# Kernel tuning notes

Hardware: AMD Instinct MI355X
Metric: run time of the kernel (lower is better)

## Reference

```python
import jax, jax.numpy as jnp
import numpy as np

B, G, D, N_HEADS, FFN, L = 16, 2048, 256, 8, 1024, 4
HEAD_DIM = D // N_HEADS
EPS_LN = 1e-5
MASK_TOKEN = -10.0
REE_BASE = 100.0


def setup_inputs() -> dict:
    key = jax.random.key(0)
    ks = jax.random.split(key, 20)
    s = 0.02
    inp = {
        'x': jax.random.normal(ks[0], (B, G), jnp.float32),
        'gene_emb': jax.random.normal(ks[1], (G, D), jnp.float32) * s,
        'inv_freq': (1.0 / REE_BASE ** (jnp.arange(0, D, 2, dtype=jnp.float32) / D)),
        'Wq': jax.random.normal(ks[2], (L, D, D), jnp.float32) * s,
        'bq': jnp.zeros((L, D), jnp.float32),
        'Wk': jax.random.normal(ks[3], (L, D, D), jnp.float32) * s,
        'bk': jnp.zeros((L, D), jnp.float32),
        'Wv': jax.random.normal(ks[4], (L, D, D), jnp.float32) * s,
        'bv': jnp.zeros((L, D), jnp.float32),
        'ln1_g': jnp.ones((L, D), jnp.float32),
        'ln1_b': jnp.zeros((L, D), jnp.float32),
        'ln2_g': jnp.ones((L, D), jnp.float32),
        'ln2_b': jnp.zeros((L, D), jnp.float32),
        'WU': jax.random.normal(ks[5], (L, D, FFN), jnp.float32) * s,
        'bU': jnp.zeros((L, FFN), jnp.float32),
        'WV': jax.random.normal(ks[6], (L, FFN, D), jnp.float32) * s,
        'bV': jnp.zeros((L, D), jnp.float32),
        'Wout': jax.random.normal(ks[7], (D, 1), jnp.float32) * s,
        'bout': jnp.zeros((1,), jnp.float32),
    }
    return inp


def layernorm(x, g, b):
    m = x.mean(-1, keepdims=True)
    v = ((x - m) ** 2).mean(-1, keepdims=True)
    return (x - m) / jnp.sqrt(v + EPS_LN) * g + b


def causal_linear_attention(q, k, v):
    # q, k already feature-mapped ('sqr'); shapes [B, S, H, dh]
    b, s, h, dh = q.shape
    qs, ks_, vs = (jnp.moveaxis(t, 1, 0) for t in (q, k, v))  # [S,B,H,dh]
    num0 = jnp.zeros((b, h, dh, dh), q.dtype)
    den0 = jnp.zeros((b, h, dh), q.dtype)

    def step(carry, qkv):
        num_s, den_s = carry
        qt, kt, vt = qkv
        num_s = num_s + jnp.einsum('bhf,bhd->bhfd', kt, vt)
        den_s = den_s + kt
        num = jnp.einsum('bhf,bhfd->bhd', qt, num_s)
        den = jnp.einsum('bhf,bhf->bh', qt, den_s)
        return (num_s, den_s), num / (den[..., None] + 1e-16)

    _, out = jax.lax.scan(step, (num0, den0), (qs, ks_, vs))  # [S,B,H,dh]
    return jnp.moveaxis(out, 0, 1).reshape(b, s, h * dh)


def reference(x, gene_emb, inv_freq, Wq, bq, Wk, bk, Wv, bv,
              ln1_g, ln1_b, ln2_g, ln2_b, WU, bU, WV, bV, Wout, bout):
    b, g = x.shape
    # Rotary Expression Embedding
    freqs = x[..., None] * inv_freq  # [B,G,D/2]
    emb = jnp.concatenate([jnp.sin(freqs), jnp.cos(freqs)], axis=-1)  # [B,G,D]
    emb = jnp.where((x == MASK_TOKEN)[..., None], 0.0, emb)
    h = gene_emb[None] + emb  # [B,G,D]

    for l in range(Wq.shape[0]):
        hn = layernorm(h, ln1_g[l], ln1_b[l])  # pre-LN (on_gptln=True)
        q = (hn @ Wq[l] + bq[l]).reshape(b, g, N_HEADS, HEAD_DIM) ** 2
        k = (hn @ Wk[l] + bk[l]).reshape(b, g, N_HEADS, HEAD_DIM) ** 2
        v = (hn @ Wv[l] + bv[l]).reshape(b, g, N_HEADS, HEAD_DIM)
        h = h + causal_linear_attention(q, k, v)
        hn2 = layernorm(h, ln2_g[l], ln2_b[l])
        h = h + jax.nn.gelu(hn2 @ WU[l] + bU[l], approximate=False) @ WV[l] + bV[l]
    return (h @ Wout + bout).squeeze(-1)  # [B,G]
```

## Files before the change

kernel.cpp:

```cpp
#include <hip/hip_runtime.h>
#include <math.h>


#define GG 2048
#define DD 256
#define NROWS 32768
#define NC 32
#define CS 64

typedef __attribute__((ext_vector_type(8))) short bf16x8;
typedef __attribute__((ext_vector_type(4))) float f32x4;

struct FalseT { static constexpr bool value = false; };
struct TrueT  { static constexpr bool value = true;  };

__device__ __forceinline__ short f2bf(float f) {
  union { float f; unsigned u; } v; v.f = f;
  unsigned r = v.u + 0x7FFFu + ((v.u >> 16) & 1u);
  return (short)(r >> 16);
}
__device__ __forceinline__ float bf2f(short s) {
  union { unsigned u; float f; } v; v.u = ((unsigned)(unsigned short)s) << 16;
  return v.f;
}
__device__ __forceinline__ void gld16(const short* g, short* l) {
  __builtin_amdgcn_global_load_lds(
      (const __attribute__((address_space(1))) void*)g,
      (__attribute__((address_space(3))) void*)l, 16, 0, 0);
}
__device__ __forceinline__ float fast_gelu(float x) {
  float y = 1.595769122f * (x + 0.044715f * x * x * x);
  return x / (1.0f + __expf(-y));
}

__global__ __launch_bounds__(256) void embed_kernel(
    const float* __restrict__ x, const float* __restrict__ ge,
    const float* __restrict__ invf, float* __restrict__ h) {
  int bg = blockIdx.x * 4 + (threadIdx.x >> 6);
  int g = bg & (GG - 1);
  int lane = threadIdx.x & 63;
  float xv = x[bg];
  int d = lane * 4;
  float4 e;
  if (lane < 32) {
    float4 f = *(const float4*)&invf[d];
    e.x = sinf(xv * f.x); e.y = sinf(xv * f.y);
    e.z = sinf(xv * f.z); e.w = sinf(xv * f.w);
  } else {
    float4 f = *(const float4*)&invf[d - 128];
    e.x = cosf(xv * f.x); e.y = cosf(xv * f.y);
    e.z = cosf(xv * f.z); e.w = cosf(xv * f.w);
  }
  if (xv == -10.0f) { e.x = 0.f; e.y = 0.f; e.z = 0.f; e.w = 0.f; }
  float4 gv = *(const float4*)&ge[(size_t)g * DD + d];
  float4 o; o.x = gv.x + e.x; o.y = gv.y + e.y; o.z = gv.z + e.z; o.w = gv.w + e.w;
  *(float4*)&h[(size_t)bg * DD + d] = o;
}

__global__ __launch_bounds__(256) void ln_tiled(
    const float* __restrict__ h, const float* __restrict__ gamma,
    const float* __restrict__ beta, short* __restrict__ outT) {
  __shared__ float mean_s[32], rstd_s[32];
  __shared__ float gls[256], bls[256];
  int r0 = blockIdx.x * 32;
  int tid = threadIdx.x;
  gls[tid] = gamma[tid]; bls[tid] = beta[tid];
  {
    int row = tid >> 3, seg = tid & 7;
    const float4* hp = (const float4*)(h + (size_t)(r0 + row) * DD + seg * 32);
    float s = 0.f, s2 = 0.f;
#pragma unroll
    for (int i = 0; i < 8; ++i) {
      float4 v = hp[i];
      s += v.x + v.y + v.z + v.w;
      s2 += v.x * v.x + v.y * v.y + v.z * v.z + v.w * v.w;
    }
    s += __shfl_xor(s, 1); s += __shfl_xor(s, 2); s += __shfl_xor(s, 4);
    s2 += __shfl_xor(s2, 1); s2 += __shfl_xor(s2, 2); s2 += __shfl_xor(s2, 4);
    if (seg == 0) {
      float mn = s * (1.0f / 256.0f);
      mean_s[row] = mn;
      rstd_s[row] = rsqrtf(s2 * (1.0f / 256.0f) - mn * mn + 1e-5f);
    }
  }
  __syncthreads();
  int row = tid & 31, kc8 = (tid >> 5) & 3, half = tid >> 7;
  float mn = mean_s[row], rs = rstd_s[row];
  size_t hrow = (size_t)(r0 + row) * DD;
  int trow = (r0 & 127) + row;
  short* tb = outT + (size_t)(r0 >> 7) * 8 * 4096 + (kc8 * 128 + trow) * 8;
#pragma unroll
  for (int j = 0; j < 4; ++j) {
    int kb = half * 4 + j;
    int k0 = kb * 32 + kc8 * 8;
    float4 x0 = *(const float4*)&h[hrow + k0];
    float4 x1 = *(const float4*)&h[hrow + k0 + 4];
    float4 g0 = *(const float4*)&gls[k0], g1 = *(const float4*)&gls[k0 + 4];
    float4 b0 = *(const float4*)&bls[k0], b1 = *(const float4*)&bls[k0 + 4];
    bf16x8 aw;
    aw[0] = f2bf((x0.x - mn) * rs * g0.x + b0.x);
    aw[1] = f2bf((x0.y - mn) * rs * g0.y + b0.y);
    aw[2] = f2bf((x0.z - mn) * rs * g0.z + b0.z);
    aw[3] = f2bf((x0.w - mn) * rs * g0.w + b0.w);
    aw[4] = f2bf((x1.x - mn) * rs * g1.x + b1.x);
    aw[5] = f2bf((x1.y - mn) * rs * g1.y + b1.y);
    aw[6] = f2bf((x1.z - mn) * rs * g1.z + b1.z);
    aw[7] = f2bf((x1.w - mn) * rs * g1.w + b1.w);
    *(bf16x8*)&tb[(size_t)kb * 4096] = aw;
  }
}

__global__ __launch_bounds__(256) void prep_weights(
    const float* __restrict__ Wq, const float* __restrict__ Wk,
    const float* __restrict__ Wv, const float* __restrict__ WU,
    const float* __restrict__ WV,
    short* __restrict__ TQ, short* __restrict__ TK, short* __restrict__ TV,
    short* __restrict__ TU, short* __restrict__ TVd) {
  int zz = blockIdx.z, l = blockIdx.y;
  const float* src; short* dst; int Kd, Nd;
  if (zz == 0) { src = Wq; dst = TQ; Kd = 256; Nd = 256; }
  else if (zz == 1) { src = Wk; dst = TK; Kd = 256; Nd = 256; }
  else if (zz == 2) { src = Wv; dst = TV; Kd = 256; Nd = 256; }
  else if (zz == 3) { src = WU; dst = TU; Kd = 256; Nd = 1024; }
  else { src = WV; dst = TVd; Kd = 1024; Nd = 256; }
  int tot = Kd * Nd;
  int e = blockIdx.x * 256 + threadIdx.x;
  if (e >= tot) return;
  int t = e >> 12;
  int cslot = (e >> 3) & 511;
  int elem = e & 7;
  int kc8 = cslot >> 7, rn = cslot & 127;
  int nKb = Kd >> 5;
  int nt = t / nKb, kb = t - nt * nKb;
  int n = nt * 128 + rn, k = kb * 32 + kc8 * 8 + elem;
  dst[(size_t)l * tot + e] = f2bf(src[(size_t)l * tot + (size_t)k * Nd + n]);
}

template <int K, int EPI>
__global__ __launch_bounds__(256) void gemm_t(
    const short* __restrict__ A, const short* __restrict__ B0,
    const short* __restrict__ B1, const short* __restrict__ B2,
    const float* __restrict__ bias0, const float* __restrict__ bias1,
    const float* __restrict__ bias2,
    short* __restrict__ o0, short* __restrict__ o1, short* __restrict__ o2,
    float* __restrict__ outf, int N) {
  __shared__ __align__(16) short L[24576];
  constexpr int nIter = K / 32;
  int z = blockIdx.z;
  const short* Bt = (z == 0) ? B0 : (z == 1) ? B1 : B2;
  const float* bias = (z == 0) ? bias0 : (z == 1) ? bias1 : bias2;
  short* outz = (z == 0) ? o0 : (z == 1) ? o1 : o2;
  int m0 = blockIdx.x * 128, n0 = blockIdx.y * 128;
  int tid = threadIdx.x;
  int lane = tid & 63, w = tid >> 6;
  int q = lane >> 4, r = lane & 15;
  int wm = (w >> 1) * 64, wn = (w & 1) * 64;
  const short* At = A + (size_t)blockIdx.x * nIter * 4096;
  const short* Btl = Bt + (size_t)blockIdx.y * nIter * 4096;
  f32x4 vzero = {0.f, 0.f, 0.f, 0.f};
  f32x4 acc[4][4];
#pragma unroll
  for (int i = 0; i < 4; ++i)
#pragma unroll
    for (int j = 0; j < 4; ++j) acc[i][j] = vzero;

  int c0 = tid * 8, c1 = (tid + 256) * 8;
#pragma unroll
  for (int g = 0; g < 3; ++g) {
    gld16(At + g * 4096 + c0, &L[g * 4096 + c0]);
    gld16(At + g * 4096 + c1, &L[g * 4096 + c1]);
    gld16(Btl + g * 4096 + c0, &L[12288 + g * 4096 + c0]);
    gld16(Btl + g * 4096 + c1, &L[12288 + g * 4096 + c1]);
  }

  int abase = (q * 128 + wm + r) * 8;
  int bbase = (q * 128 + wn + r) * 8;

#pragma unroll
  for (int gi = 0; gi < nIter; ++gi) {
    const int rem = nIter - 1 - gi;
    if (rem >= 2)      __builtin_amdgcn_s_waitcnt(0x0f78);
    else if (rem == 1) __builtin_amdgcn_s_waitcnt(0x0f74);
    else               __builtin_amdgcn_s_waitcnt(0x0f70);
    __builtin_amdgcn_s_barrier();
    const int cur = gi % 3;
    const short* Asc = &L[cur * 4096];
    const short* Bsc = &L[12288 + cur * 4096];
    bf16x8 af[4], bfr[4];
#pragma unroll
    for (int mt = 0; mt < 4; ++mt)
      af[mt] = *(const bf16x8*)&Asc[abase + mt * 16 * 8];
#pragma unroll
    for (int nt = 0; nt < 4; ++nt)
      bfr[nt] = *(const bf16x8*)&Bsc[bbase + nt * 16 * 8];
#pragma unroll
    for (int mt = 0; mt < 4; ++mt)
#pragma unroll
      for (int nt = 0; nt < 4; ++nt)
        acc[mt][nt] = __builtin_amdgcn_mfma_f32_16x16x32_bf16(bfr[nt], af[mt], acc[mt][nt], 0, 0, 0);
    __builtin_amdgcn_s_waitcnt(0xc07f);
    __builtin_amdgcn_s_barrier();
    if (gi + 3 < nIter) {
      size_t kn = (size_t)(gi + 3) * 4096;
      gld16(At + kn + c0, &L[cur * 4096 + c0]);
      gld16(At + kn + c1, &L[cur * 4096 + c1]);
      gld16(Btl + kn + c0, &L[12288 + cur * 4096 + c0]);
      gld16(Btl + kn + c1, &L[12288 + cur * 4096 + c1]);
    }
  }

  float4 bias4[4];
#pragma unroll
  for (int nt = 0; nt < 4; ++nt) bias4[nt] = *(const float4*)&bias[n0 + wn + nt * 16 + q * 4];

  if (EPI == 0) {
    short* T = L;
#pragma unroll
    for (int mt = 0; mt < 4; ++mt) {
      int ml = wm + mt * 16 + r;
#pragma unroll
      for (int nt = 0; nt < 4; ++nt) {
        f32x4 v = acc[mt][nt];
        v[0] += bias4[nt].x; v[1] += bias4[nt].y; v[2] += bias4[nt].z; v[3] += bias4[nt].w;
        if (z < 2) { v[0] *= v[0]; v[1] *= v[1]; v[2] *= v[2]; v[3] *= v[3]; }
        short4 pk; pk.x = f2bf(v[0]); pk.y = f2bf(v[1]); pk.z = f2bf(v[2]); pk.w = f2bf(v[3]);
        *(short4*)&T[ml * 132 + wn + nt * 16 + q * 4] = pk;
      }
    }
    __syncthreads();
#pragma unroll
    for (int t2 = 0; t2 < 2; ++t2) {
      int task = tid + t2 * 256;
      int row = task & 127, hl = task >> 7;
      size_t obase = ((size_t)((n0 >> 5) + hl) * NROWS + m0 + row) * 32;
#pragma unroll
      for (int j = 0; j < 4; ++j)
        *(bf16x8*)&outz[obase + j * 8] = *(const bf16x8*)&T[row * 132 + hl * 32 + j * 8];
    }
  } else if (EPI == 1) {
#pragma unroll
    for (int mt = 0; mt < 4; ++mt) {
      int ml = wm + mt * 16 + r;
#pragma unroll
      for (int nt = 0; nt < 4; ++nt) {
        f32x4 v = acc[mt][nt];
        v[0] += bias4[nt].x; v[1] += bias4[nt].y; v[2] += bias4[nt].z; v[3] += bias4[nt].w;
#pragma unroll
        for (int e = 0; e < 4; ++e) v[e] = fast_gelu(v[e]);
        short4 o; o.x = f2bf(v[0]); o.y = f2bf(v[1]); o.z = f2bf(v[2]); o.w = f2bf(v[3]);
        int n = n0 + wn + nt * 16 + q * 4;
        size_t ti = ((size_t)blockIdx.x * (N >> 5) + (n >> 5)) * 4096 +
                    (size_t)(((n >> 3) & 3) << 10) + (ml << 3) + (n & 7);
        *(short4*)&outz[ti] = o;
      }
    }
  } else {
    float* TF = (float*)L;
#pragma unroll
    for (int half = 0; half < 2; ++half) {
      __syncthreads();
      if ((w & 1) == half) {
#pragma unroll
        for (int mt = 0; mt < 4; ++mt) {
          int ml = wm + mt * 16 + r;
#pragma unroll
          for (int nt = 0; nt < 4; ++nt) {
            f32x4 v = acc[mt][nt];
            v[0] += bias4[nt].x; v[1] += bias4[nt].y; v[2] += bias4[nt].z; v[3] += bias4[nt].w;
            *(f32x4*)&TF[ml * 68 + nt * 16 + q * 4] = v;
          }
        }
      }
      __syncthreads();
      int row = tid >> 1, col = (tid & 1) * 32;
      size_t hoff = (size_t)(m0 + row) * N + n0 + half * 64 + col;
#pragma unroll
      for (int j = 0; j < 8; ++j) {
        float4 add = *(const float4*)&TF[row * 68 + col + j * 4];
        float4 cur4 = *(float4*)&outf[hoff + j * 4];
        cur4.x += add.x; cur4.y += add.y; cur4.z += add.z; cur4.w += add.w;
        *(float4*)&outf[hoff + j * 4] = cur4;
      }
    }
  }
}

__global__ __launch_bounds__(512) void ffn_fused(
    const short* __restrict__ A, const short* __restrict__ TUw,
    const short* __restrict__ TVw, const float* __restrict__ bUp,
    const float* __restrict__ bVp, float* __restrict__ h) {
  __shared__ __align__(16) short L[75776];
  float* BU = (float*)&L[73728];
  int tid = threadIdx.x;
  int lane = tid & 63, w = tid >> 6;
  int q = lane >> 4, r = lane & 15;
  int wmU = (w >> 1) * 32, wnU = (w & 1) * 64;
  int wmD = (w >> 2) * 64, wnD = (w & 3) * 64;
  int c16 = tid * 8;
  const short* At = A + (size_t)blockIdx.x * 32768;

  if (tid < 256) *(float4*)&BU[tid * 4] = *(const float4*)&bUp[tid * 4];

#pragma unroll
  for (int i = 0; i < 8; ++i) gld16(At + i * 4096 + c16, &L[i * 4096 + c16]);

  auto issueUp = [&](int ss, int jj, int buf) {
    short* dst = &L[49152 + buf * 8192];
    const short* g0 = TUw + ((size_t)ss * 8 + jj * 2) * 4096;
    gld16(g0 + c16, dst + c16);
    gld16(g0 + 4096 + c16, dst + 4096 + c16);
  };
  auto issueDown = [&](int ss, int ii, int buf) {
    short* dst = &L[49152 + buf * 8192];
    gld16(TVw + (size_t)(ss * 4 + ii) * 4096 + c16, dst + c16);
    gld16(TVw + (size_t)(32 + ss * 4 + ii) * 4096 + c16, dst + 4096 + c16);
  };

  issueUp(0, 0, 0); issueUp(0, 1, 1); issueUp(0, 2, 2);

  __builtin_amdgcn_s_waitcnt(0x0f76);
  __builtin_amdgcn_s_barrier();

  bf16x8 aR[8][2];
#pragma unroll
  for (int kb = 0; kb < 8; ++kb)
#pragma unroll
    for (int mt = 0; mt < 2; ++mt)
      aR[kb][mt] = *(const bf16x8*)&L[kb * 4096 + (q * 128 + wmU + mt * 16 + r) * 8];

  f32x4 vzero = {0.f, 0.f, 0.f, 0.f};
  f32x4 accm[2][4], acco[4][4];
#pragma unroll
  for (int mt = 0; mt < 2; ++mt)
#pragma unroll
    for (int nt = 0; nt < 4; ++nt) accm[mt][nt] = vzero;
#pragma unroll
  for (int mt = 0; mt < 4; ++mt)
#pragma unroll
    for (int nt = 0; nt < 4; ++nt) acco[mt][nt] = vzero;

  int cur = 0;

  auto slice = [&](int s, auto lastc) {
    constexpr bool LAST = decltype(lastc)::value;
#pragma unroll
    for (int j = 0; j < 4; ++j) {
      __builtin_amdgcn_s_waitcnt(0x0f74);
      __builtin_amdgcn_s_barrier();
      const short* Ws = &L[49152 + cur * 8192];
#pragma unroll
      for (int kk = 0; kk < 2; ++kk) {
        bf16x8 bfr[4];
#pragma unroll
        for (int nt = 0; nt < 4; ++nt)
          bfr[nt] = *(const bf16x8*)&Ws[kk * 4096 + (q * 128 + wnU + nt * 16 + r) * 8];
#pragma unroll
        for (int mt = 0; mt < 2; ++mt)
#pragma unroll
          for (int nt = 0; nt < 4; ++nt)
            accm[mt][nt] = __builtin_amdgcn_mfma_f32_16x16x32_bf16(
                bfr[nt], aR[j * 2 + kk][mt], accm[mt][nt], 0, 0, 0);
      }
      if (j == 3) {
        float4 b4[4];
#pragma unroll
        for (int nt = 0; nt < 4; ++nt)
          b4[nt] = *(const float4*)&BU[s * 128 + wnU + nt * 16 + q * 4];
#pragma unroll
        for (int mt = 0; mt < 2; ++mt) {
          int row = wmU + mt * 16 + r;
#pragma unroll
          for (int nt = 0; nt < 4; ++nt) {
            f32x4 v = accm[mt][nt];
            v[0] += b4[nt].x; v[1] += b4[nt].y; v[2] += b4[nt].z; v[3] += b4[nt].w;
            short4 pk;
            pk.x = f2bf(fast_gelu(v[0])); pk.y = f2bf(fast_gelu(v[1]));
            pk.z = f2bf(fast_gelu(v[2])); pk.w = f2bf(fast_gelu(v[3]));
            int f0 = wnU + nt * 16 + q * 4;
            *(short4*)&L[32768 + (f0 >> 5) * 4096 +
                         (((f0 >> 3) & 3) * 128 + row) * 8 + (f0 & 7)] = pk;
            accm[mt][nt] = vzero;
          }
        }
      }
      __builtin_amdgcn_s_waitcnt(0xc07f);
      __builtin_amdgcn_s_barrier();
      if (j == 0) issueUp(s, 3, cur);
      else issueDown(s, j - 1, cur);
      cur = (cur == 2) ? 0 : cur + 1;
    }
#pragma unroll
    for (int i = 0; i < 4; ++i) {
      if (LAST && i == 2)      __builtin_amdgcn_s_waitcnt(0x0f72);
      else if (LAST && i == 3) __builtin_amdgcn_s_waitcnt(0x0f70);
      else                     __builtin_amdgcn_s_waitcnt(0x0f74);
      __builtin_amdgcn_s_barrier();
      const short* Ws = &L[49152 + cur * 8192];
      bf16x8 am[4], bvf[4];
#pragma unroll
      for (int mt = 0; mt < 4; ++mt)
        am[mt] = *(const bf16x8*)&L[32768 + i * 4096 + (q * 128 + wmD + mt * 16 + r) * 8];
#pragma unroll
      for (int nt = 0; nt < 4; ++nt)
        bvf[nt] = *(const bf16x8*)&Ws[(wnD >> 7) * 4096 + (q * 128 + (wnD & 127) + nt * 16 + r) * 8];
#pragma unroll
      for (int mt = 0; mt < 4; ++mt)
#pragma unroll
        for (int nt = 0; nt < 4; ++nt)
          acco[mt][nt] = __builtin_amdgcn_mfma_f32_16x16x32_bf16(bvf[nt], am[mt], acco[mt][nt], 0, 0, 0);
      __builtin_amdgcn_s_waitcnt(0xc07f);
      __builtin_amdgcn_s_barrier();
      if (i == 0) issueDown(s, 3, cur);
      else if (!LAST) issueUp(s + 1, i - 1, cur);
      cur = (cur == 2) ? 0 : cur + 1;
    }
  };

  for (int s = 0; s < 7; ++s) slice(s, FalseT{});
  slice(7, TrueT{});

  float4 bv4[4];
#pragma unroll
  for (int nt = 0; nt < 4; ++nt) bv4[nt] = *(const float4*)&bVp[wnD + nt * 16 + q * 4];
  float* TF = (float*)L;
#pragma unroll
  for (int mt = 0; mt < 4; ++mt) {
    int row = wmD + mt * 16 + r;
#pragma unroll
    for (int nt = 0; nt < 4; ++nt) {
      f32x4 v = acco[mt][nt];
      v[0] += bv4[nt].x; v[1] += bv4[nt].y; v[2] += bv4[nt].z; v[3] += bv4[nt].w;
      *(f32x4*)&TF[row * 260 + wnD + nt * 16 + q * 4] = v;
    }
  }
  __syncthreads();
  size_t hbase = ((size_t)blockIdx.x * 128 + w * 16) * DD;
#pragma unroll
  for (int j = 0; j < 16; ++j) {
    float4 add = *(const float4*)&TF[(w * 16 + j) * 260 + lane * 4];
    float4 c4 = *(float4*)&h[hbase + (size_t)j * DD + lane * 4];
    c4.x += add.x; c4.y += add.y; c4.z += add.z; c4.w += add.w;
    *(float4*)&h[hbase + (size_t)j * DD + lane * 4] = c4;
  }
}

__global__ __launch_bounds__(256) void attn_chunk_kv(
    const short* __restrict__ Kb, const short* __restrict__ Vb,
    float* __restrict__ St, float* __restrict__ Zc) {
  __shared__ short Kt[4][32 * 72];
  __shared__ short Vt[4][32 * 72];
  int wid = threadIdx.x >> 6;
  int blk = blockIdx.x * 4 + wid;
  int c = blk & (NC - 1), bh = blk >> 5;
  int b = bh >> 3, hh = bh & 7;
  int lane = threadIdx.x & 63, q = lane >> 4, r = lane & 15;
  size_t rowbase = ((size_t)hh * NROWS + b * GG + c * CS + lane) * 32;
#pragma unroll
  for (int j = 0; j < 4; ++j) {
    bf16x8 kv = *(const bf16x8*)&Kb[rowbase + j * 8];
    bf16x8 vv = *(const bf16x8*)&Vb[rowbase + j * 8];
#pragma unroll
    for (int e = 0; e < 8; ++e) {
      Kt[wid][(j * 8 + e) * 72 + lane] = kv[e];
      Vt[wid][(j * 8 + e) * 72 + lane] = vv[e];
    }
  }
  __syncthreads();
  f32x4 vzero = {0.f, 0.f, 0.f, 0.f};
  f32x4 acc[2][2];
#pragma unroll
  for (int i = 0; i < 2; ++i)
#pragma unroll
    for (int j = 0; j < 2; ++j) acc[i][j] = vzero;
#pragma unroll
  for (int ks = 0; ks < 2; ++ks) {
    bf16x8 afr[2], bfr[2];
#pragma unroll
    for (int mt = 0; mt < 2; ++mt) afr[mt] = *(const bf16x8*)&Kt[wid][(mt * 16 + r) * 72 + ks * 32 + q * 8];
#pragma unroll
    for (int nt = 0; nt < 2; ++nt) bfr[nt] = *(const bf16x8*)&Vt[wid][(nt * 16 + r) * 72 + ks * 32 + q * 8];
#pragma unroll
    for (int mt = 0; mt < 2; ++mt)
#pragma unroll
      for (int nt = 0; nt < 2; ++nt)
        acc[mt][nt] = __builtin_amdgcn_mfma_f32_16x16x32_bf16(afr[mt], bfr[nt], acc[mt][nt], 0, 0, 0);
  }
  float* stp = St + ((size_t)bh * NC + c) * 1024;
#pragma unroll
  for (int mt = 0; mt < 2; ++mt)
#pragma unroll
    for (int nt = 0; nt < 2; ++nt)
      *(f32x4*)&stp[(nt * 16 + r) * 32 + mt * 16 + q * 4] = acc[mt][nt];
  if (lane < 32) {
    float s = 0.f;
#pragma unroll
    for (int j = 0; j < 8; ++j) {
      bf16x8 kr = *(const bf16x8*)&Kt[wid][lane * 72 + j * 8];
#pragma unroll
      for (int e = 0; e < 8; ++e) s += bf2f(kr[e]);
    }
    Zc[((size_t)bh * NC + c) * 32 + lane] = s;
  }
}

__global__ __launch_bounds__(1024) void attn_prefix(float* __restrict__ St, float* __restrict__ Zc) {
  int bh = blockIdx.x, i = threadIdx.x;
  float run = 0.f;
  float* p = St + (size_t)bh * NC * 1024 + i;
#pragma unroll
  for (int c = 0; c < NC; ++c) { float t = p[(size_t)c * 1024]; p[(size_t)c * 1024] = run; run += t; }
  if (i < 32) {
    float rz = 0.f;
    float* pz = Zc + (size_t)bh * NC * 32 + i;
#pragma unroll
    for (int c = 0; c < NC; ++c) { float t = pz[c * 32]; pz[c * 32] = rz; rz += t; }
  }
}

__global__ __launch_bounds__(256) void attn_intra(
    const short* __restrict__ Qb, const short* __restrict__ Kb,
    const short* __restrict__ Vb, const float* __restrict__ St,
    const float* __restrict__ Zc, float* __restrict__ h) {
  __shared__ short P[4][64 * 72];
  __shared__ short Vt[4][32 * 72];
  __shared__ float den[4][64];
  int wid = threadIdx.x >> 6;
  int blk = blockIdx.x * 4 + wid;
  int c = blk & (NC - 1), bh = blk >> 5;
  int b = bh >> 3, hh = bh & 7;
  int lane = threadIdx.x & 63, q = lane >> 4, r = lane & 15;
  size_t hrow0 = (size_t)b * GG + c * CS;
  size_t qrow0 = (size_t)hh * NROWS + b * GG + c * CS;

  const float* zp = Zc + ((size_t)bh * NC + c) * 32;
  float qz = 0.f;
  {
    size_t qoff = (qrow0 + lane) * 32;
#pragma unroll
    for (int j = 0; j < 4; ++j) {
      bf16x8 qv = *(const bf16x8*)&Qb[qoff + j * 8];
#pragma unroll
      for (int e = 0; e < 8; ++e) qz += bf2f(qv[e]) * zp[j * 8 + e];
    }
  }
  den[wid][lane] = qz;

  {
    size_t voff = (qrow0 + lane) * 32;
#pragma unroll
    for (int j = 0; j < 4; ++j) {
      bf16x8 vv = *(const bf16x8*)&Vb[voff + j * 8];
#pragma unroll
      for (int e = 0; e < 8; ++e) Vt[wid][(j * 8 + e) * 72 + lane] = vv[e];
    }
  }

  bf16x8 ak[4], bqf[4];
#pragma unroll
  for (int t4 = 0; t4 < 4; ++t4) {
    ak[t4]  = *(const bf16x8*)&Kb[(qrow0 + t4 * 16 + r) * 32 + q * 8];
    bqf[t4] = *(const bf16x8*)&Qb[(qrow0 + t4 * 16 + r) * 32 + q * 8];
  }
  f32x4 vzero = {0.f, 0.f, 0.f, 0.f};
  f32x4 pacc[4][4];
#pragma unroll
  for (int mt = 0; mt < 4; ++mt)
#pragma unroll
    for (int nt = 0; nt < 4; ++nt)
      pacc[mt][nt] = __builtin_amdgcn_mfma_f32_16x16x32_bf16(ak[mt], bqf[nt], vzero, 0, 0, 0);

  float rs[4] = {0.f, 0.f, 0.f, 0.f};
#pragma unroll
  for (int nt = 0; nt < 4; ++nt) {
    int t = nt * 16 + r;
#pragma unroll
    for (int mt = 0; mt < 4; ++mt) {
      short4 pk;
#pragma unroll
      for (int rr = 0; rr < 4; ++rr) {
        int s = mt * 16 + q * 4 + rr;
        float pv = (s <= t) ? pacc[mt][nt][rr] : 0.f;
        rs[nt] += pv;
        ((short*)&pk)[rr] = f2bf(pv);
      }
      *(short4*)&P[wid][t * 72 + mt * 16 + q * 4] = pk;
    }
  }
#pragma unroll
  for (int nt = 0; nt < 4; ++nt) {
    rs[nt] += __shfl_xor(rs[nt], 16);
    rs[nt] += __shfl_xor(rs[nt], 32);
  }
  __syncthreads();
  if (lane < 16) {
#pragma unroll
    for (int nt = 0; nt < 4; ++nt) den[wid][nt * 16 + lane] += rs[nt];
  }
  __syncthreads();

  f32x4 oacc[4][2];
#pragma unroll
  for (int mt = 0; mt < 4; ++mt)
#pragma unroll
    for (int nt2 = 0; nt2 < 2; ++nt2) oacc[mt][nt2] = vzero;
  const float* stp = St + ((size_t)bh * NC + c) * 1024;
#pragma unroll
  for (int nt2 = 0; nt2 < 2; ++nt2) {
    float4 s0 = *(const float4*)&stp[(nt2 * 16 + r) * 32 + q * 8];
    float4 s1 = *(const float4*)&stp[(nt2 * 16 + r) * 32 + q * 8 + 4];
    bf16x8 bs;
    bs[0] = f2bf(s0.x); bs[1] = f2bf(s0.y); bs[2] = f2bf(s0.z); bs[3] = f2bf(s0.w);
    bs[4] = f2bf(s1.x); bs[5] = f2bf(s1.y); bs[6] = f2bf(s1.z); bs[7] = f2bf(s1.w);
#pragma unroll
    for (int mt = 0; mt < 4; ++mt)
      oacc[mt][nt2] = __builtin_amdgcn_mfma_f32_16x16x32_bf16(bqf[mt], bs, oacc[mt][nt2], 0, 0, 0);
  }
#pragma unroll
  for (int ks = 0; ks < 2; ++ks) {
    bf16x8 ap[4];
#pragma unroll
    for (int mt = 0; mt < 4; ++mt)
      ap[mt] = *(const bf16x8*)&P[wid][(mt * 16 + r) * 72 + ks * 32 + q * 8];
#pragma unroll
    for (int nt2 = 0; nt2 < 2; ++nt2) {
      bf16x8 bv_ = *(const bf16x8*)&Vt[wid][(nt2 * 16 + r) * 72 + ks * 32 + q * 8];
#pragma unroll
      for (int mt = 0; mt < 4; ++mt)
        oacc[mt][nt2] = __builtin_amdgcn_mfma_f32_16x16x32_bf16(ap[mt], bv_, oacc[mt][nt2], 0, 0, 0);
    }
  }

#pragma unroll
  for (int mt = 0; mt < 4; ++mt) {
#pragma unroll
    for (int rr = 0; rr < 4; ++rr) {
      int t = mt * 16 + q * 4 + rr;
      float inv = 1.0f / (den[wid][t] + 1e-16f);
#pragma unroll
      for (int nt2 = 0; nt2 < 2; ++nt2) {
        int d = nt2 * 16 + r;
        size_t off = (hrow0 + t) * DD + hh * 32 + d;
        h[off] += oacc[mt][nt2][rr] * inv;
      }
    }
  }
}

__global__ __launch_bounds__(256) void out_proj(
    const float* __restrict__ h, const float* __restrict__ Wout,
    const float* __restrict__ bout, float* __restrict__ out) {
  int row = blockIdx.x * 4 + (threadIdx.x >> 6);
  int lane = threadIdx.x & 63;
  float4 a = *(const float4*)&h[(size_t)row * DD + lane * 4];
  float4 w = *(const float4*)&Wout[lane * 4];
  float s = a.x * w.x + a.y * w.y + a.z * w.z + a.w * w.w;
#pragma unroll
  for (int o = 1; o < 64; o <<= 1) s += __shfl_xor(s, o);
  if (lane == 0) out[row] = s + bout[0];
}

extern "C" void kernel_launch(void* const* d_in, const int* in_sizes, int n_in,
                              void* d_out, int out_size, void* d_ws, size_t ws_size,
                              hipStream_t stream) {
  const float* x    = (const float*)d_in[0];
  const float* ge   = (const float*)d_in[1];
  const float* invf = (const float*)d_in[2];
  const float* Wq   = (const float*)d_in[3];
  const float* bq   = (const float*)d_in[4];
  const float* Wk   = (const float*)d_in[5];
  const float* bk   = (const float*)d_in[6];
  const float* Wv   = (const float*)d_in[7];
  const float* bv   = (const float*)d_in[8];
  const float* ln1g = (const float*)d_in[9];
  const float* ln1b = (const float*)d_in[10];
  const float* ln2g = (const float*)d_in[11];
  const float* ln2b = (const float*)d_in[12];
  const float* WU   = (const float*)d_in[13];
  const float* bU   = (const float*)d_in[14];
  const float* WV   = (const float*)d_in[15];
  const float* bV   = (const float*)d_in[16];
  const float* Wout = (const float*)d_in[17];
  const float* bout = (const float*)d_in[18];
  float* out = (float*)d_out;

  char* ws = (char*)d_ws;
  float* h   = (float*)(ws + 0);
  short* hn  = (short*)(ws + 33554432);
  char*  R   = ws + 50331648;
  short* qb  = (short*)(R + 0);
  short* kb  = (short*)(R + 16777216);
  short* vb  = (short*)(R + 33554432);
  float* St  = (float*)(R + 50331648);
  float* Zc  = (float*)(R + 67108864);
  char*  WT  = R + 67633152;
  short* TQ  = (short*)(WT + 0);
  short* TK  = (short*)(WT + 524288);
  short* TVq = (short*)(WT + 1048576);
  short* TU  = (short*)(WT + 1572864);
  short* TVd = (short*)(WT + 3670016);

  prep_weights<<<dim3(1024, 4, 5), 256, 0, stream>>>(Wq, Wk, Wv, WU, WV, TQ, TK, TVq, TU, TVd);
  embed_kernel<<<NROWS / 4, 256, 0, stream>>>(x, ge, invf, h);

  for (int l = 0; l < 4; ++l) {
    ln_tiled<<<NROWS / 32, 256, 0, stream>>>(h, ln1g + l * 256, ln1b + l * 256, hn);
    gemm_t<256, 0><<<dim3(256, 2, 3), 256, 0, stream>>>(
        hn, TQ + l * 65536, TK + l * 65536, TVq + l * 65536,
        bq + l * 256, bk + l * 256, bv + l * 256,
        qb, kb, vb, nullptr, 256);
    attn_chunk_kv<<<1024, 256, 0, stream>>>(kb, vb, St, Zc);
    attn_prefix<<<128, 1024, 0, stream>>>(St, Zc);
    attn_intra<<<1024, 256, 0, stream>>>(qb, kb, vb, St, Zc, h);
    ln_tiled<<<NROWS / 32, 256, 0, stream>>>(h, ln2g + l * 256, ln2b + l * 256, hn);
    ffn_fused<<<256, 512, 0, stream>>>(hn, TU + l * 262144, TVd + l * 262144,
                                       bU + l * 1024, bV + l * 256, h);
  }
  out_proj<<<NROWS / 4, 256, 0, stream>>>(h, Wout, bout, out);
}
```

Measured before the change: 753.8 us.

## Split fused FFN into 64-row blocks of 256 threads with smaller LDS

The fused FFN kernel now processes 64 rows per block with 4 waves instead of 128 rows with 8 waves, launching 512 blocks instead of 256. Activations are loaded straight from global memory into registers instead of being staged through LDS, and the LDS footprint drops from about 148KB to about 68KB. This should allow more blocks per CU and fill all CUs, but each weight slice is now streamed twice as often per row processed. Each wave also holds a larger 2x8 down-projection tile, which raises register pressure.

```diff
diff --git a/kernel.cpp b/kernel.cpp
--- a/kernel.cpp
+++ b/kernel.cpp
@@ -285,59 +285,60 @@
   }
 }
 
-__global__ __launch_bounds__(512) void ffn_fused(
+__global__ __launch_bounds__(256) void ffn_fused(
     const short* __restrict__ A, const short* __restrict__ TUw,
     const short* __restrict__ TVw, const float* __restrict__ bUp,
     const float* __restrict__ bVp, float* __restrict__ h) {
-  __shared__ __align__(16) short L[75776];
-  float* BU = (float*)&L[73728];
+  __shared__ __align__(16) short L[34816];
+  float* BU = (float*)&L[32768];
   int tid = threadIdx.x;
   int lane = tid & 63, w = tid >> 6;
   int q = lane >> 4, r = lane & 15;
   int wmU = (w >> 1) * 32, wnU = (w & 1) * 64;
-  int wmD = (w >> 2) * 64, wnD = (w & 3) * 64;
-  int c16 = tid * 8;
-  const short* At = A + (size_t)blockIdx.x * 32768;
-
-  if (tid < 256) *(float4*)&BU[tid * 4] = *(const float4*)&bUp[tid * 4];
-
-#pragma unroll
-  for (int i = 0; i < 8; ++i) gld16(At + i * 4096 + c16, &L[i * 4096 + c16]);
+  int wmD = (w >> 1) * 32, wnD = (w & 1) * 128;
+  const short* At = A + (size_t)(blockIdx.x >> 1) * 32768;
+  int rbase = (blockIdx.x & 1) * 64;
+
+  *(float4*)&BU[tid * 4] = *(const float4*)&bUp[tid * 4];
+
+  bf16x8 aR[8][2];
+#pragma unroll
+  for (int kb = 0; kb < 8; ++kb)
+#pragma unroll
+    for (int mt = 0; mt < 2; ++mt)
+      aR[kb][mt] = *(const bf16x8*)&At[kb * 4096 + (q * 128 + rbase + wmU + mt * 16 + r) * 8];
+
+  __builtin_amdgcn_s_waitcnt(0x0f70);
 
   auto issueUp = [&](int ss, int jj, int buf) {
-    short* dst = &L[49152 + buf * 8192];
+    short* dst = &L[8192 + buf * 8192];
     const short* g0 = TUw + ((size_t)ss * 8 + jj * 2) * 4096;
-    gld16(g0 + c16, dst + c16);
-    gld16(g0 + 4096 + c16, dst + 4096 + c16);
+#pragma unroll
+    for (int i = 0; i < 4; ++i)
+      gld16(g0 + (i * 256 + tid) * 8, dst + (i * 256 + tid) * 8);
   };
   auto issueDown = [&](int ss, int ii, int buf) {
-    short* dst = &L[49152 + buf * 8192];
-    gld16(TVw + (size_t)(ss * 4 + ii) * 4096 + c16, dst + c16);
-    gld16(TVw + (size_t)(32 + ss * 4 + ii) * 4096 + c16, dst + 4096 + c16);
+    short* dst = &L[8192 + buf * 8192];
+    const short* gA = TVw + (size_t)(ss * 4 + ii) * 4096;
+    const short* gB = TVw + (size_t)(32 + ss * 4 + ii) * 4096;
+#pragma unroll
+    for (int i = 0; i < 2; ++i) {
+      gld16(gA + (i * 256 + tid) * 8, dst + (i * 256 + tid) * 8);
+      gld16(gB + (i * 256 + tid) * 8, dst + 4096 + (i * 256 + tid) * 8);
+    }
   };
 
   issueUp(0, 0, 0); issueUp(0, 1, 1); issueUp(0, 2, 2);
 
-  __builtin_amdgcn_s_waitcnt(0x0f76);
-  __builtin_amdgcn_s_barrier();
-
-  bf16x8 aR[8][2];
-#pragma unroll
-  for (int kb = 0; kb < 8; ++kb)
-#pragma unroll
-    for (int mt = 0; mt < 2; ++mt)
-      aR[kb][mt] = *(const bf16x8*)&L[kb * 4096 + (q * 128 + wmU + mt * 16 + r) * 8];
-
   f32x4 vzero = {0.f, 0.f, 0.f, 0.f};
-  f32x4 accm[2][4], acco[4][4];
-#pragma unroll
-  for (int mt = 0; mt < 2; ++mt)
+  f32x4 accm[2][4], acco[2][8];
+#pragma unroll
+  for (int mt = 0; mt < 2; ++mt) {
 #pragma unroll
     for (int nt = 0; nt < 4; ++nt) accm[mt][nt] = vzero;
 #pragma unroll
-  for (int mt = 0; mt < 4; ++mt)
-#pragma unroll
-    for (int nt = 0; nt < 4; ++nt) acco[mt][nt] = vzero;
+    for (int nt = 0; nt < 8; ++nt) acco[mt][nt] = vzero;
+  }
 
   int cur = 0;
 
@@ -345,9 +346,9 @@
     constexpr bool LAST = decltype(lastc)::value;
 #pragma unroll
     for (int j = 0; j < 4; ++j) {
-      __builtin_amdgcn_s_waitcnt(0x0f74);
+      __builtin_amdgcn_s_waitcnt(0x0f78);
       __builtin_amdgcn_s_barrier();
-      const short* Ws = &L[49152 + cur * 8192];
+      const short* Ws = &L[8192 + cur * 8192];
 #pragma unroll
       for (int kk = 0; kk < 2; ++kk) {
         bf16x8 bfr[4];
@@ -377,8 +378,7 @@
             pk.x = f2bf(fast_gelu(v[0])); pk.y = f2bf(fast_gelu(v[1]));
             pk.z = f2bf(fast_gelu(v[2])); pk.w = f2bf(fast_gelu(v[3]));
             int f0 = wnU + nt * 16 + q * 4;
-            *(short4*)&L[32768 + (f0 >> 5) * 4096 +
-                         (((f0 >> 3) & 3) * 128 + row) * 8 + (f0 & 7)] = pk;
+            *(short4*)&L[(f0 >> 5) * 2048 + (((f0 >> 3) & 3) * 64 + row) * 8 + (f0 & 7)] = pk;
             accm[mt][nt] = vzero;
           }
         }
@@ -391,22 +391,22 @@
     }
 #pragma unroll
     for (int i = 0; i < 4; ++i) {
-      if (LAST && i == 2)      __builtin_amdgcn_s_waitcnt(0x0f72);
+      if (LAST && i == 2)      __builtin_amdgcn_s_waitcnt(0x0f74);
       else if (LAST && i == 3) __builtin_amdgcn_s_waitcnt(0x0f70);
-      else                     __builtin_amdgcn_s_waitcnt(0x0f74);
+      else                     __builtin_amdgcn_s_waitcnt(0x0f78);
       __builtin_amdgcn_s_barrier();
-      const short* Ws = &L[49152 + cur * 8192];
-      bf16x8 am[4], bvf[4];
-#pragma unroll
-      for (int mt = 0; mt < 4; ++mt)
-        am[mt] = *(const bf16x8*)&L[32768 + i * 4096 + (q * 128 + wmD + mt * 16 + r) * 8];
-#pragma unroll
-      for (int nt = 0; nt < 4; ++nt)
+      const short* Ws = &L[8192 + cur * 8192];
+      bf16x8 am[2], bvf[8];
+#pragma unroll
+      for (int mt = 0; mt < 2; ++mt)
+        am[mt] = *(const bf16x8*)&L[i * 2048 + (q * 64 + wmD + mt * 16 + r) * 8];
+#pragma unroll
+      for (int nt = 0; nt < 8; ++nt)
         bvf[nt] = *(const bf16x8*)&Ws[(wnD >> 7) * 4096 + (q * 128 + (wnD & 127) + nt * 16 + r) * 8];
 #pragma unroll
-      for (int mt = 0; mt < 4; ++mt)
-#pragma unroll
-        for (int nt = 0; nt < 4; ++nt)
+      for (int mt = 0; mt < 2; ++mt)
+#pragma unroll
+        for (int nt = 0; nt < 8; ++nt)
           acco[mt][nt] = __builtin_amdgcn_mfma_f32_16x16x32_bf16(bvf[nt], am[mt], acco[mt][nt], 0, 0, 0);
       __builtin_amdgcn_s_waitcnt(0xc07f);
       __builtin_amdgcn_s_barrier();
@@ -419,28 +419,29 @@
   for (int s = 0; s < 7; ++s) slice(s, FalseT{});
   slice(7, TrueT{});
 
-  float4 bv4[4];
-#pragma unroll
-  for (int nt = 0; nt < 4; ++nt) bv4[nt] = *(const float4*)&bVp[wnD + nt * 16 + q * 4];
+  float4 bv4[8];
+#pragma unroll
+  for (int nt = 0; nt < 8; ++nt) bv4[nt] = *(const float4*)&bVp[wnD + nt * 16 + q * 4];
   float* TF = (float*)L;
 #pragma unroll
-  for (int mt = 0; mt < 4; ++mt) {
+  for (int mt = 0; mt < 2; ++mt) {
     int row = wmD + mt * 16 + r;
 #pragma unroll
-    for (int nt = 0; nt < 4; ++nt) {
+    for (int nt = 0; nt < 8; ++nt) {
       f32x4 v = acco[mt][nt];
       v[0] += bv4[nt].x; v[1] += bv4[nt].y; v[2] += bv4[nt].z; v[3] += bv4[nt].w;
       *(f32x4*)&TF[row * 260 + wnD + nt * 16 + q * 4] = v;
     }
   }
   __syncthreads();
-  size_t hbase = ((size_t)blockIdx.x * 128 + w * 16) * DD;
+  int row2 = tid >> 2, col2 = (tid & 3) * 64;
+  size_t hbase = ((size_t)blockIdx.x * 64 + row2) * DD + col2;
 #pragma unroll
   for (int j = 0; j < 16; ++j) {
-    float4 add = *(const float4*)&TF[(w * 16 + j) * 260 + lane * 4];
-    float4 c4 = *(float4*)&h[hbase + (size_t)j * DD + lane * 4];
+    float4 add = *(const float4*)&TF[row2 * 260 + col2 + j * 4];
+    float4 c4 = *(float4*)&h[hbase + j * 4];
     c4.x += add.x; c4.y += add.y; c4.z += add.z; c4.w += add.w;
-    *(float4*)&h[hbase + (size_t)j * DD + lane * 4] = c4;
+    *(float4*)&h[hbase + j * 4] = c4;
   }
 }
 
@@ -712,7 +713,7 @@
     attn_prefix<<<128, 1024, 0, stream>>>(St, Zc);
     attn_intra<<<1024, 256, 0, stream>>>(qb, kb, vb, St, Zc, h);
     ln_tiled<<<NROWS / 32, 256, 0, stream>>>(h, ln2g + l * 256, ln2b + l * 256, hn);
-    ffn_fused<<<256, 512, 0, stream>>>(hn, TU + l * 262144, TVd + l * 262144,
+    ffn_fused<<<512, 256, 0, stream>>>(hn, TU + l * 262144, TVd + l * 262144,
                                        bU + l * 1024, bV + l * 256, h);
   }
   out_proj<<<NROWS / 4, 256, 0, stream>>>(h, Wout, bout, out);
```

Measured after the change: 930.1 us. +23.4%, slower.
